# Optimization experiments

Measured on AMD Instinct MI355X. Metric: run time of the kernel, lower is better.

## Reference

```python
import jax, jax.numpy as jnp
import numpy as np

WINDOW_SIZE = 7
C1 = 0.01 ** 2
C2 = 0.03 ** 2


def _gaussian_window(ws: int) -> jnp.ndarray:
    sigma = ws / 6.0
    coords = jnp.arange(ws, dtype=jnp.float32) - ws // 2
    g = jnp.exp(-coords ** 2 / (2 * sigma ** 2))
    g = g / g.sum()
    k3 = g[:, None, None] * g[None, :, None] * g[None, None, :]
    k3 = k3 / k3.sum()
    return k3.reshape(1, 1, ws, ws, ws)  # OIDHW


def _conv3d_same(x, w):
    pad = WINDOW_SIZE // 2
    return jax.lax.conv_general_dilated(
        x, w, window_strides=(1, 1, 1),
        padding=[(pad, pad)] * 3,
        dimension_numbers=('NCDHW', 'OIDHW', 'NCDHW'))


def setup_inputs() -> dict:
    key = jax.random.key(0)
    k1, k2 = jax.random.split(key)
    shape = (2, 1, 160, 160, 160)
    predicted = jax.random.uniform(k1, shape, dtype=jnp.float32)
    target = jax.random.uniform(k2, shape, dtype=jnp.float32)
    return {"predicted": predicted, "target": target}


def reference(predicted, target):
    window = _gaussian_window(WINDOW_SIZE)
    mu1 = _conv3d_same(predicted, window)
    mu2 = _conv3d_same(target, window)
    mu1_sq = mu1 ** 2
    mu2_sq = mu2 ** 2
    mu1_mu2 = mu1 * mu2
    sigma1_sq = _conv3d_same(predicted ** 2, window) - mu1_sq
    sigma2_sq = _conv3d_same(target ** 2, window) - mu2_sq
    sigma12 = _conv3d_same(predicted * target, window) - mu1_mu2
    ssim_map = ((2 * mu1_mu2 + C1) * (2 * sigma12 + C2)) / (
        (mu1_sq + mu2_sq + C1) * (sigma1_sq + sigma2_sq + C2))
    return 1.0 - ssim_map.mean()
```

## Files before the change

### kernel.cpp

```cpp
#include <hip/hip_runtime.h>
#include <math.h>

#define DD 160
#define HH 160
#define WW 160
#define NB 2
#define NEL (NB*DD*HH*WW)

#define XT 32
#define YT 16
#define ZC 16
#define NTHR 256
#define NZCH (DD/ZC)
#define GX (WW/XT)
#define GY (HH/YT)
#define NPART (GX*GY*NB*NZCH)

#define HR 22
#define NJOB (HR*8)
#define CP 35

typedef float v2f __attribute__((ext_vector_type(2)));

struct G7 { float g[7]; };

__global__ __launch_bounds__(NTHR, 4) void ssim_fused(
        const float* __restrict__ p, const float* __restrict__ t,
        float* __restrict__ partial, G7 gw) {
    const int tid = threadIdx.x;
    const int tx  = tid & 31;
    const int tyo = tid >> 5;
    const int x0 = blockIdx.x * XT;
    const int y0 = blockIdx.y * YT;
    const int n  = blockIdx.z / NZCH;
    const int zs = (blockIdx.z % NZCH) * ZC;

    __shared__ float4 c4[2][HR][CP];

    v2f r01[2][6], r23[2][6];
#pragma unroll
    for (int yo = 0; yo < 2; ++yo)
#pragma unroll
        for (int j = 0; j < 6; ++j) {
            r01[yo][j] = (v2f)(0.f);
            r23[yo][j] = (v2f)(0.f);
        }

    const float C1v = 1e-4f, C2v = 9e-4f;
    float ssum = 0.f;
    const int hw = HH * WW;
    const float* pv = p + (size_t)n * DD * hw;
    const float* tv = t + (size_t)n * DD * hw;

    const int br = tid >> 3;
    const int bxg = tid & 7;
    const int bgy = y0 + br - 3;
    const bool browok = (unsigned)bgy < (unsigned)HH && tid < NJOB;
    const int cbase = x0 + 4 * bxg - 4;
    const int pcr = tx + (tx >> 3);

    for (int s = zs - 3; s < zs + ZC + 3; ++s) {
        const int par = s & 1;
        v2f m01[2], m23[2];
#pragma unroll
        for (int yo = 0; yo < 2; ++yo) {
            m01[yo] = (v2f)(0.f);
            m23[yo] = (v2f)(0.f);
        }

        const bool valid = (s >= 0) && (s < DD);
        if (valid) {
            if (tid < NJOB) {
                const float* prow = pv + (size_t)s * hw + bgy * WW;
                const float* trow = tv + (size_t)s * hw + bgy * WW;
                v2f s01[4], s23[4];
#pragma unroll
                for (int e = 0; e < 4; ++e) { s01[e] = (v2f)(0.f); s23[e] = (v2f)(0.f); }
#pragma unroll
                for (int q = 0; q < 3; ++q) {
                    int c0 = cbase + 4 * q;
                    float4 a = make_float4(0.f, 0.f, 0.f, 0.f);
                    float4 b = a;
                    if (browok && (unsigned)c0 < (unsigned)WW) {
                        a = *(const float4*)(prow + c0);
                        b = *(const float4*)(trow + c0);
                    }
                    const float af[4] = {a.x, a.y, a.z, a.w};
                    const float bf[4] = {b.x, b.y, b.z, b.w};
#pragma unroll
                    for (int j = 0; j < 4; ++j) {
                        const int i = 4 * q + j;
                        v2f pt; pt[0] = af[j]; pt[1] = bf[j];
                        v2f ud; ud[0] = af[j] + bf[j]; ud[1] = af[j] - bf[j];
                        v2f qu = ud * ud;
#pragma unroll
                        for (int e = 0; e < 4; ++e) {
                            const int k = i - e - 1;
                            if (k >= 0 && k < 7) {
                                s01[e] = gw.g[k] * pt + s01[e];
                                s23[e] = gw.g[k] * qu + s23[e];
                            }
                        }
                    }
                }
#pragma unroll
                for (int e = 0; e < 4; ++e) {
                    int c = 4 * bxg + e;
                    c4[par][br][c + (c >> 3)] =
                        make_float4(s01[e][0], s01[e][1], s23[e][0], s23[e][1]);
                }
            }
            __syncthreads();

#pragma unroll
            for (int r8 = 0; r8 < 8; ++r8) {
                float4 v = c4[par][2 * tyo + r8][pcr];
                v2f v01; v01[0] = v.x; v01[1] = v.y;
                v2f v23; v23[0] = v.z; v23[1] = v.w;
                if (r8 < 7) {
                    float w = gw.g[r8];
                    m01[0] = w * v01 + m01[0];
                    m23[0] = w * v23 + m23[0];
                }
                if (r8 > 0) {
                    float w = gw.g[r8 - 1];
                    m01[1] = w * v01 + m01[1];
                    m23[1] = w * v23 + m23[1];
                }
            }
        }

#pragma unroll
        for (int yo = 0; yo < 2; ++yo) {
            v2f v01 = m01[yo], v23 = m23[yo];
            v2f cons01 = gw.g[6] * v01 + r01[yo][0];
            v2f cons23 = gw.g[6] * v23 + r23[yo][0];
#pragma unroll
            for (int j = 0; j < 5; ++j) {
                r01[yo][j] = gw.g[5 - j] * v01 + r01[yo][j + 1];
                r23[yo][j] = gw.g[5 - j] * v23 + r23[yo][j + 1];
            }
            r01[yo][5] = gw.g[0] * v01;
            r23[yo][5] = gw.g[0] * v23;

            if (s >= zs + 3) {
                float mu1 = cons01[0], mu2 = cons01[1];
                float Eu  = cons23[0], Ew  = cons23[1];
                float mu12 = mu1 * mu2, mu1sq = mu1 * mu1, mu2sq = mu2 * mu2;
                float sumsq = 0.5f  * (Eu + Ew) - mu1sq - mu2sq;
                float s12   = 0.25f * (Eu - Ew) - mu12;
                float num = (2.f * mu12 + C1v) * (2.f * s12 + C2v);
                float den = (mu1sq + mu2sq + C1v) * (sumsq + C2v);
                ssum += num * __builtin_amdgcn_rcpf(den);
            }
        }
    }

#pragma unroll
    for (int off = 32; off > 0; off >>= 1)
        ssum += __shfl_down(ssum, off, 64);
    __shared__ float wsum[4];
    if ((tid & 63) == 0) wsum[tid >> 6] = ssum;
    __syncthreads();
    if (tid == 0) {
        int bid = (blockIdx.z * GY + blockIdx.y) * GX + blockIdx.x;
        partial[bid] = wsum[0] + wsum[1] + wsum[2] + wsum[3];
    }
}

__global__ __launch_bounds__(256) void ssim_final(
        const float* __restrict__ partial, float* __restrict__ out) {
    float s = 0.f;
    for (int i = threadIdx.x; i < NPART; i += 256) s += partial[i];
#pragma unroll
    for (int off = 32; off > 0; off >>= 1)
        s += __shfl_down(s, off, 64);
    __shared__ float wsum[4];
    int lane = threadIdx.x & 63, wid = threadIdx.x >> 6;
    if (lane == 0) wsum[wid] = s;
    __syncthreads();
    if (threadIdx.x == 0) {
        float tot = wsum[0] + wsum[1] + wsum[2] + wsum[3];
        out[0] = 1.0f - tot / (float)NEL;
    }
}

extern "C" void kernel_launch(void* const* d_in, const int* in_sizes, int n_in,
                              void* d_out, int out_size, void* d_ws, size_t ws_size,
                              hipStream_t stream) {
    const float* p = (const float*)d_in[0];
    const float* t = (const float*)d_in[1];
    float* out = (float*)d_out;
    float* partial = (float*)d_ws;

    G7 gw;
    {
        double s = 0.0, sig = 7.0 / 6.0;
        double g[7];
        for (int i = 0; i < 7; ++i) {
            double d = (double)i - 3.0;
            g[i] = exp(-d * d / (2.0 * sig * sig));
            s += g[i];
        }
        for (int i = 0; i < 7; ++i) gw.g[i] = (float)(g[i] / s);
    }

    dim3 grid(GX, GY, NB * NZCH);
    ssim_fused<<<grid, NTHR, 0, stream>>>(p, t, partial, gw);
    ssim_final<<<1, 256, 0, stream>>>(partial, out);
}
```

Measured before the change: 132.4 us.

## Prefetch next z-slice into registers and remap blocks across XCDs

Loads for slice s+1 are now issued into registers right after the shared-memory write barrier, so global-memory latency overlaps the y-convolution and z-recurrence of the current slice. The grid is flattened to 1D and block indices are permuted so that consecutive hardware-dispatched blocks (round-robin across the 8 XCDs) map to contiguous spatial tiles on each XCD, aiming to improve L2 reuse of halo rows. The prefetch adds register pressure (24 floats), which could lower occupancy under the launch bounds.

```diff
diff --git a/kernel.cpp b/kernel.cpp
--- a/kernel.cpp
+++ b/kernel.cpp
@@ -14,7 +14,8 @@
 #define NZCH (DD/ZC)
 #define GX (WW/XT)
 #define GY (HH/YT)
-#define NPART (GX*GY*NB*NZCH)
+#define NBLK (GX*GY*NB*NZCH)
+#define NPART NBLK
 
 #define HR 22
 #define NJOB (HR*8)
@@ -30,10 +31,17 @@
     const int tid = threadIdx.x;
     const int tx  = tid & 31;
     const int tyo = tid >> 5;
-    const int x0 = blockIdx.x * XT;
-    const int y0 = blockIdx.y * YT;
-    const int n  = blockIdx.z / NZCH;
-    const int zs = (blockIdx.z % NZCH) * ZC;
+
+    const int flat = blockIdx.x;
+    const int w = (flat & 7) * (NBLK / 8) + (flat >> 3);
+    const int bx = w % GX;
+    const int by = (w / GX) % GY;
+    const int bz = w / (GX * GY);
+
+    const int x0 = bx * XT;
+    const int y0 = by * YT;
+    const int n  = bz / NZCH;
+    const int zs = (bz % NZCH) * ZC;
 
     __shared__ float4 c4[2][HR][CP];
 
@@ -59,34 +67,42 @@
     const int cbase = x0 + 4 * bxg - 4;
     const int pcr = tx + (tx >> 3);
 
+    float4 pfa[3], pfb[3];
+    auto prefetch = [&](int sx) {
+#pragma unroll
+        for (int q = 0; q < 3; ++q) {
+            pfa[q] = make_float4(0.f, 0.f, 0.f, 0.f);
+            pfb[q] = make_float4(0.f, 0.f, 0.f, 0.f);
+        }
+        if (browok && sx >= 0 && sx < DD && sx < zs + ZC + 3) {
+            const float* prow = pv + (size_t)sx * hw + bgy * WW;
+            const float* trow = tv + (size_t)sx * hw + bgy * WW;
+#pragma unroll
+            for (int q = 0; q < 3; ++q) {
+                int c0 = cbase + 4 * q;
+                if ((unsigned)c0 < (unsigned)WW) {
+                    pfa[q] = *(const float4*)(prow + c0);
+                    pfb[q] = *(const float4*)(trow + c0);
+                }
+            }
+        }
+    };
+
+    prefetch(zs - 3);
+
     for (int s = zs - 3; s < zs + ZC + 3; ++s) {
         const int par = s & 1;
-        v2f m01[2], m23[2];
-#pragma unroll
-        for (int yo = 0; yo < 2; ++yo) {
-            m01[yo] = (v2f)(0.f);
-            m23[yo] = (v2f)(0.f);
-        }
-
         const bool valid = (s >= 0) && (s < DD);
+
         if (valid) {
             if (tid < NJOB) {
-                const float* prow = pv + (size_t)s * hw + bgy * WW;
-                const float* trow = tv + (size_t)s * hw + bgy * WW;
                 v2f s01[4], s23[4];
 #pragma unroll
                 for (int e = 0; e < 4; ++e) { s01[e] = (v2f)(0.f); s23[e] = (v2f)(0.f); }
 #pragma unroll
                 for (int q = 0; q < 3; ++q) {
-                    int c0 = cbase + 4 * q;
-                    float4 a = make_float4(0.f, 0.f, 0.f, 0.f);
-                    float4 b = a;
-                    if (browok && (unsigned)c0 < (unsigned)WW) {
-                        a = *(const float4*)(prow + c0);
-                        b = *(const float4*)(trow + c0);
-                    }
-                    const float af[4] = {a.x, a.y, a.z, a.w};
-                    const float bf[4] = {b.x, b.y, b.z, b.w};
+                    const float af[4] = {pfa[q].x, pfa[q].y, pfa[q].z, pfa[q].w};
+                    const float bf[4] = {pfb[q].x, pfb[q].y, pfb[q].z, pfb[q].w};
 #pragma unroll
                     for (int j = 0; j < 4; ++j) {
                         const int i = 4 * q + j;
@@ -111,21 +127,32 @@
                 }
             }
             __syncthreads();
-
+        }
+
+        prefetch(s + 1);
+
+        v2f m01[2], m23[2];
+#pragma unroll
+        for (int yo = 0; yo < 2; ++yo) {
+            m01[yo] = (v2f)(0.f);
+            m23[yo] = (v2f)(0.f);
+        }
+
+        if (valid) {
 #pragma unroll
             for (int r8 = 0; r8 < 8; ++r8) {
                 float4 v = c4[par][2 * tyo + r8][pcr];
                 v2f v01; v01[0] = v.x; v01[1] = v.y;
                 v2f v23; v23[0] = v.z; v23[1] = v.w;
                 if (r8 < 7) {
-                    float w = gw.g[r8];
-                    m01[0] = w * v01 + m01[0];
-                    m23[0] = w * v23 + m23[0];
+                    float w2 = gw.g[r8];
+                    m01[0] = w2 * v01 + m01[0];
+                    m23[0] = w2 * v23 + m23[0];
                 }
                 if (r8 > 0) {
-                    float w = gw.g[r8 - 1];
-                    m01[1] = w * v01 + m01[1];
-                    m23[1] = w * v23 + m23[1];
+                    float w2 = gw.g[r8 - 1];
+                    m01[1] = w2 * v01 + m01[1];
+                    m23[1] = w2 * v23 + m23[1];
                 }
             }
         }
@@ -162,10 +189,8 @@
     __shared__ float wsum[4];
     if ((tid & 63) == 0) wsum[tid >> 6] = ssum;
     __syncthreads();
-    if (tid == 0) {
-        int bid = (blockIdx.z * GY + blockIdx.y) * GX + blockIdx.x;
-        partial[bid] = wsum[0] + wsum[1] + wsum[2] + wsum[3];
-    }
+    if (tid == 0)
+        partial[flat] = wsum[0] + wsum[1] + wsum[2] + wsum[3];
 }
 
 __global__ __launch_bounds__(256) void ssim_final(
@@ -205,7 +230,6 @@
         for (int i = 0; i < 7; ++i) gw.g[i] = (float)(g[i] / s);
     }
 
-    dim3 grid(GX, GY, NB * NZCH);
-    ssim_fused<<<grid, NTHR, 0, stream>>>(p, t, partial, gw);
+    ssim_fused<<<NBLK, NTHR, 0, stream>>>(p, t, partial, gw);
     ssim_final<<<1, 256, 0, stream>>>(partial, out);
 }
```

After: 128.3 us. 1.03x faster.
